# Kernel optimization log

Hardware: AMD Instinct MI355X
Metric: run time of the kernel (lower is better)

## Reference

```python
import jax, jax.numpy as jnp
import numpy as np

EPS = 0.5
MIN_SAMPLES = 5


def setup_inputs() -> dict:
    key = jax.random.key(0)
    X = jax.random.uniform(key, (12288, 8), dtype=jnp.float32)
    return {"X": X}


def reference(X):
    """DBSCAN: eps-range queries + cluster expansion, expressed as
    eps-graph connected components over core points (same clustering
    as the serial BFS in the original module; cluster ids are assigned
    in order of each cluster's minimum core index, matching the
    ascending-scan discovery order of the original)."""
    N = X.shape[0]
    SENTINEL = jnp.int32(N)

    # pairwise squared Euclidean distances [N, N] (KDTree range query equivalent)
    sq = jnp.sum(X * X, axis=1)
    d2 = sq[:, None] + sq[None, :] - 2.0 * (X @ X.T)
    adj = d2 <= (EPS * EPS)                      # eps-neighborhood (includes self)

    density = jnp.sum(adj, axis=1)               # |query_ball_point(x_i, eps)|
    core = density >= MIN_SAMPLES                # core-point mask

    # core-core edges: BFS expansion only propagates through cores
    core_adj = adj & core[None, :] & core[:, None]

    idx = jnp.arange(N, dtype=jnp.int32)
    init = jnp.where(core, idx, SENTINEL)        # each core starts as its own root

    def prop(lbl):
        # min label over core neighbors (min-plus propagation = connected components)
        nb_min = jnp.min(jnp.where(core_adj, lbl[None, :], SENTINEL), axis=1)
        return jnp.minimum(lbl, nb_min)

    def cond(state):
        cur, prev = state
        return jnp.any(cur != prev)

    def body(state):
        cur, _ = state
        return prop(cur), cur

    lbl, _ = jax.lax.while_loop(cond, body, (prop(init), init))

    # border points: non-core points within eps of a core join that core's cluster
    core_nb = jnp.min(jnp.where(adj & core[None, :], lbl[None, :], SENTINEL), axis=1)
    root = jnp.where(core, lbl, core_nb)         # SENTINEL -> noise

    # compact cluster ids: rank of each cluster root (min core index) ascending,
    # matching the original's sequential discovery order k = 0, 1, ...
    is_root = core & (lbl == idx)
    rank = jnp.cumsum(is_root.astype(jnp.int32)) - 1   # rank[i] valid where is_root[i]
    labels = jnp.where(root < SENTINEL,
                       rank[jnp.clip(root, 0, N - 1)],
                       jnp.int32(-1))
    return labels
```

## Files before the change

### kernel.cpp

```cpp
#include <hip/hip_runtime.h>

#define NPTS 12288
#define DIMS 8
#define EPS2 0.25f
#define MINS 5
#define NIB1 (NPTS / 256)
#define NW   (NPTS / 32)
#define SENT NPTS
#define RMAX 512
#define W    (RMAX / 32)
#define BIGL 0x3fffffff
#define FT   128
#define FB   256
#define FBGRID 256

#define ATHR 256
#define AROWS 2
#define ATI  (ATHR * AROWS)
#define AJC  128
#define AWCH (AJC / 32)
#define NJC  (NPTS / AJC)
#define NBLK 1200

typedef float v2f __attribute__((ext_vector_type(2)));

__device__ __forceinline__ float dot8(const v2f* xi, const float4& a, const float4& b) {
  v2f y0 = {a.x, a.y}, y1 = {a.z, a.w}, y2 = {b.x, b.y}, y3 = {b.z, b.w};
  v2f d = xi[0] * y0;
  d = __builtin_elementwise_fma(xi[1], y1, d);
  d = __builtin_elementwise_fma(xi[2], y2, d);
  d = __builtin_elementwise_fma(xi[3], y3, d);
  return d.x + d.y;
}

__device__ __forceinline__ unsigned int tr32(unsigned int x, int lane31) {
  const unsigned int M[5] = {0x0000FFFFu, 0x00FF00FFu, 0x0F0F0F0Fu,
                             0x33333333u, 0x55555555u};
  const int S[5] = {16, 8, 4, 2, 1};
#pragma unroll
  for (int k = 0; k < 5; ++k) {
    int s = S[k];
    unsigned int m = M[k];
    unsigned int p = __shfl_xor(x, s, 32);
    x = (lane31 & s) ? ((x & ~m) | ((p >> s) & m))
                     : ((x & m) | ((p & m) << s));
  }
  return x;
}


__global__ __launch_bounds__(ATHR) void k_adj(const float* __restrict__ X,
                                              unsigned int* __restrict__ adj,
                                              int* __restrict__ density) {
  __shared__ float4 xs[AJC][2];
  __shared__ float sqs[AJC];
  __shared__ unsigned int mir[AJC * 17];
  int t = threadIdx.x;

  int B = blockIdx.x;
  int bx = 0;
  while (2 * (bx + 1) * (48 - bx) <= B) bx++;
  int by = 4 * bx + (B - 2 * bx * (49 - bx));
  bool full = (by >= 4 * bx + 4);

  if (t < AJC) {
    int j = by * AJC + t;
    float4 a = ((const float4*)X)[j * 2];
    float4 b = ((const float4*)X)[j * 2 + 1];
    xs[t][0] = a; xs[t][1] = b;
    float sv = 0.f;
    sv = fmaf(a.x, a.x, sv); sv = fmaf(a.y, a.y, sv); sv = fmaf(a.z, a.z, sv); sv = fmaf(a.w, a.w, sv);
    sv = fmaf(b.x, b.x, sv); sv = fmaf(b.y, b.y, sv); sv = fmaf(b.z, b.z, sv); sv = fmaf(b.w, b.w, sv);
    sqs[t] = sv;
  }
  int i0 = bx * ATI + t, i1 = i0 + ATHR;
  v2f xi0[4], xi1[4];
  {
    float4 a0 = ((const float4*)X)[i0 * 2], b0v = ((const float4*)X)[i0 * 2 + 1];
    float4 a1 = ((const float4*)X)[i1 * 2], b1v = ((const float4*)X)[i1 * 2 + 1];
    xi0[0] = (v2f){a0.x, a0.y}; xi0[1] = (v2f){a0.z, a0.w};
    xi0[2] = (v2f){b0v.x, b0v.y}; xi0[3] = (v2f){b0v.z, b0v.w};
    xi1[0] = (v2f){a1.x, a1.y}; xi1[1] = (v2f){a1.z, a1.w};
    xi1[2] = (v2f){b1v.x, b1v.y}; xi1[3] = (v2f){b1v.z, b1v.w};
  }
  float sq0 = 0.f, sq1 = 0.f;
#pragma unroll
  for (int q = 0; q < 4; q++) {
    v2f p0 = xi0[q] * xi0[q], p1 = xi1[q] * xi1[q];
    sq0 += p0.x + p0.y; sq1 += p1.x + p1.y;
  }
  __syncthreads();
  unsigned int acc0[AWCH], acc1[AWCH];
#pragma unroll
  for (int w = 0; w < AWCH; w++) {
    unsigned int b0 = 0u, b1 = 0u;
#pragma unroll 4
    for (int bit = 0; bit < 32; bit++) {
      int jj = (w << 5) + bit;
      float4 xa = xs[jj][0], xb = xs[jj][1];
      float sj = sqs[jj];
      unsigned int m = 1u << bit;
      float d20 = (sq0 + sj) - 2.0f * dot8(xi0, xa, xb);
      float d21 = (sq1 + sj) - 2.0f * dot8(xi1, xa, xb);
      if (d20 <= EPS2) b0 |= m;
      if (d21 <= EPS2) b1 |= m;
    }
    acc0[w] = b0; acc1[w] = b1;
  }

  if (full) {
    *(uint4*)(adj + (size_t)i0 * NW + by * AWCH) = make_uint4(acc0[0], acc0[1], acc0[2], acc0[3]);
    *(uint4*)(adj + (size_t)i1 * NW + by * AWCH) = make_uint4(acc1[0], acc1[1], acc1[2], acc1[3]);
    int pc0 = 0, pc1 = 0;
#pragma unroll
    for (int w = 0; w < AWCH; w++) { pc0 += __popc(acc0[w]); pc1 += __popc(acc1[w]); }
    atomicAdd(&density[i0], pc0);
    atomicAdd(&density[i1], pc1);
  } else {
    int lw0 = min(max((i0 >> 5) - 4 * by, 0), 4);
    int lw1 = min(max((i1 >> 5) - 4 * by, 0), 4);
    unsigned int* dst0 = adj + (size_t)i0 * NW + by * AWCH;
    unsigned int* dst1 = adj + (size_t)i1 * NW + by * AWCH;
    int pc0 = 0, pc1 = 0;
    for (int wl = lw0; wl < AWCH; wl++) { dst0[wl] = acc0[wl]; pc0 += __popc(acc0[wl]); }
    for (int wl = lw1; wl < AWCH; wl++) { dst1[wl] = acc1[wl]; pc1 += __popc(acc1[wl]); }
    if (lw0 < AWCH) atomicAdd(&density[i0], pc0);
    if (lw1 < AWCH) atomicAdd(&density[i1], pc1);
  }

  const int lane31 = t & 31;
  const int g = t >> 5;
#pragma unroll
  for (int wl = 0; wl < AWCH; ++wl) {
    unsigned int x0 = tr32(acc0[wl], lane31);
    unsigned int x1 = tr32(acc1[wl], lane31);
    int rr = (wl << 5) + lane31;
    mir[rr * 17 + g] = x0;
    mir[rr * 17 + 8 + g] = x1;
  }
  __syncthreads();
  {
    int r = t >> 1, half = t & 1;
    int rglob = by * AJC + r;
    const unsigned int* mrow = &mir[r * 17 + half * 8];
    unsigned int* dstm = adj + (size_t)rglob * NW + bx * 16 + half * 8;
    if (full) {
      ((uint4*)dstm)[0] = make_uint4(mrow[0], mrow[1], mrow[2], mrow[3]);
      ((uint4*)dstm)[1] = make_uint4(mrow[4], mrow[5], mrow[6], mrow[7]);
      int pc = 0;
#pragma unroll
      for (int q = 0; q < 8; q++) pc += __popc(mrow[q]);
      atomicAdd(&density[rglob], pc);
    } else {
      int nv = min(max((rglob >> 5) - 16 * bx, 0), 16);
      int pc = 0, st = 0;
      for (int q = 0; q < 8; q++) {
        int qg = half * 8 + q;
        if (qg < nv) { dstm[q] = mrow[q]; pc += __popc(mrow[q]); st = 1; }
      }
      if (st) atomicAdd(&density[rglob], pc);
    }
  }
}

__global__ __launch_bounds__(256) void k_core(const int* __restrict__ density,
                                              unsigned long long* __restrict__ corebm,
                                              unsigned int* __restrict__ bm) {
  int t = threadIdx.x;
  if (blockIdx.x == 0) {
#pragma unroll
    for (int q = 0; q < RMAX * W / 256; q++) bm[t + q * 256] = 0u;
  }
  int i = blockIdx.x * 256 + t;
  unsigned long long m = __ballot(density[i] >= MINS);
  if ((t & 63) == 0) corebm[i >> 6] = m;
}

__global__ __launch_bounds__(64) void k_hookbm(const unsigned int* __restrict__ adj,
                                               const unsigned int* __restrict__ cb32,
                                               int* __restrict__ hook) {
  __shared__ unsigned int cb[NW];
  int t = threadIdx.x;
  for (int w = t; w < NW; w += 64) cb[w] = cb32[w];
  __syncthreads();
  int i = blockIdx.x * 64 + t;
  const unsigned int* row = adj + (size_t)i * NW;
  int wi = i >> 5;
  int m = i;
  for (int w = 0; w <= wi; w++) {
    unsigned int x = row[w] & cb[w];
    if (w == wi) x &= (1u << (i & 31)) - 1;
    if (x) { m = (w << 5) + __ffs(x) - 1; break; }
  }
  hook[i] = m;
}

__global__ __launch_bounds__(1024) void k_rid(const int* __restrict__ density,
                                              const int* __restrict__ hook,
                                              int* __restrict__ Rptr,
                                              int* __restrict__ labL,
                                              int* __restrict__ bcount) {
  __shared__ unsigned short ridS[NPTS];
  __shared__ int wsum[16];
  int t = threadIdx.x;
  int lane = t & 63, wid = t >> 6;
  const int SEG = NPTS / 1024;
  int base = t * SEG;
  int flags = 0;
  int s = 0;
#pragma unroll
  for (int k = 0; k < SEG; k++) {
    int i = base + k;
    int f = (density[i] >= MINS && hook[i] == i) ? 1 : 0;
    flags |= f << k;
    s += f;
  }
  int segsum = s;
#pragma unroll
  for (int off = 1; off < 64; off <<= 1) {
    int n = __shfl_up(s, off, 64);
    if (lane >= off) s += n;
  }
  if (lane == 63) wsum[wid] = s;
  __syncthreads();
  int woff = 0;
  for (int w = 0; w < wid; w++) woff += wsum[w];
  int run = woff + s - segsum;
#pragma unroll
  for (int k = 0; k < SEG; k++) {
    ridS[base + k] = (unsigned short)run;
    run += (flags >> k) & 1;
  }
  if (t == 1023) *Rptr = run;
  if (t == 0) *bcount = 0;
  __syncthreads();
  for (int k = 0; k < SEG; k++) {
    int i = base + k;
    int lab = -1;
    if (density[i] >= MINS) {
      int v = i, h = hook[v];
      while (h != v) { v = h; h = hook[v]; }
      lab = min((int)ridS[v], RMAX - 1);
    }
    labL[i] = lab;
  }
}

__global__ __launch_bounds__(FB) void k_fillbm(const unsigned int* __restrict__ adj,
                                               const unsigned int* __restrict__ cb32,
                                               const int* __restrict__ labL,
                                               unsigned int* __restrict__ bm) {
  __shared__ unsigned int bmL[RMAX * W];
  __shared__ unsigned short labS[NPTS];
  __shared__ unsigned int cb[NW];
  int t = threadIdx.x;
  for (int q = t; q < RMAX * W; q += FB) bmL[q] = 0u;
  for (int q = t; q < NPTS; q += FB) labS[q] = (unsigned short)(labL[q] + 1);
  for (int w = t; w < NW; w += FB) cb[w] = cb32[w];
  __syncthreads();
  int lane = t & 63, wv = t >> 6;
  int gw = blockIdx.x * 4 + wv;
  for (int i = gw; i < NPTS; i += 4 * FBGRID) {
    int a0 = (int)labS[i] - 1;
    if (a0 < 0) continue;
    const unsigned int* row = adj + (size_t)i * NW;
    int wi = i >> 5;
    for (int w = wi + lane; w < NW; w += 64) {
      unsigned int x = row[w] & cb[w];
      if (w == wi) x &= (0xFFFFFFFEu << (i & 31));
      while (x) {
        int b = __ffs(x) - 1; x &= x - 1;
        int lj = (int)labS[(w << 5) + b] - 1;
        if (lj != a0) {
          atomicOr(&bmL[a0 * W + (lj >> 5)], 1u << (lj & 31));
          atomicOr(&bmL[lj * W + (a0 >> 5)], 1u << (a0 & 31));
        }
      }
    }
  }
  __syncthreads();
  for (int q = t; q < RMAX * W; q += FB) {
    unsigned int v = bmL[q];
    if (v) atomicOr(&bm[q], v);
  }
}

__global__ __launch_bounds__(RMAX) void k_cc(const unsigned int* __restrict__ bm,
                                             const int* __restrict__ Rptr,
                                             int* __restrict__ clab) {
  __shared__ int lbl[RMAX];
  __shared__ int mn[RMAX];
  __shared__ int chg, cmp;
  int a = threadIdx.x;
  int R = *Rptr; if (R > RMAX) R = RMAX;
  lbl[a] = a;
  __syncthreads();
  while (true) {
    int m = lbl[a];
    if (a < R) {
      const unsigned int* row = bm + a * W;
#pragma unroll
      for (int w = 0; w < W; w++) {
        unsigned int bits = row[w];
        while (bits) {
          int b = __ffs(bits) - 1;
          bits &= bits - 1;
          m = min(m, lbl[(w << 5) + b]);
        }
      }
    }
    mn[a] = m;
    if (a == 0) chg = 0;
    __syncthreads();
    int l = lbl[a];
    if (m < l) { atomicMin(&lbl[l], m); atomicMin(&lbl[a], m); chg = 1; }
    __syncthreads();
    while (true) {
      if (a == 0) cmp = 0;
      __syncthreads();
      int nl = lbl[lbl[a]];
      __syncthreads();
      if (nl < lbl[a]) { lbl[a] = nl; cmp = 1; }
      __syncthreads();
      if (!cmp) break;
    }
    if (!chg) break;
    __syncthreads();
  }
  int flag = (a < R && lbl[a] == a) ? 1 : 0;
  mn[a] = flag;
  __syncthreads();
  for (int off = 1; off < RMAX; off <<= 1) {
    int v = mn[a];
    int add = (a >= off) ? mn[a - off] : 0;
    __syncthreads();
    mn[a] = v + add;
    __syncthreads();
  }
  clab[a] = mn[lbl[a]] - 1;
}

__global__ __launch_bounds__(256) void k_labels(const int* __restrict__ labL,
                                                const int* __restrict__ clab,
                                                int* __restrict__ labArr,
                                                int* __restrict__ blist,
                                                int* __restrict__ bcount,
                                                float* __restrict__ out) {
  int i = blockIdx.x * blockDim.x + threadIdx.x;
  if (i >= NPTS) return;
  int a = labL[i];
  if (a >= 0) {
    int lab = clab[a];
    labArr[i] = lab;
    out[i] = (float)lab;
  } else {
    labArr[i] = BIGL;
    out[i] = -1.0f;
    int pos = atomicAdd(bcount, 1);
    blist[pos] = i;
  }
}

__global__ __launch_bounds__(FT) void k_border(const unsigned int* __restrict__ adj,
                                               const unsigned int* __restrict__ cb32,
                                               const int* __restrict__ labArr,
                                               const int* __restrict__ blist,
                                               const int* __restrict__ bcount,
                                               float* __restrict__ out) {
  __shared__ unsigned int cb[NW];
  __shared__ int wm[FT / 64];
  int t = threadIdx.x;
  for (int w = t; w < NW; w += FT) cb[w] = cb32[w];
  __syncthreads();
  int count = *bcount;
  for (int k = blockIdx.x; k < count; k += gridDim.x) {
    int p = blist[k];
    const unsigned int* row = adj + (size_t)p * NW;
    int m = BIGL;
    for (int w = t; w < NW; w += FT) {
      unsigned int x = row[w] & cb[w];
      while (x) {
        int b = __ffs(x) - 1; x &= x - 1;
        m = min(m, labArr[(w << 5) + b]);
      }
    }
#pragma unroll
    for (int off = 32; off >= 1; off >>= 1) m = min(m, __shfl_xor(m, off, 64));
    if ((t & 63) == 0) wm[t >> 6] = m;
    __syncthreads();
    if (t == 0) {
      int mm = min(wm[0], wm[1]);
      out[p] = (mm < BIGL) ? (float)mm : -1.0f;
    }
    __syncthreads();
  }
}


extern "C" void kernel_launch(void* const* d_in, const int* in_sizes, int n_in,
                              void* d_out, int out_size, void* d_ws, size_t ws_size,
                              hipStream_t stream) {
  const float* X = (const float*)d_in[0];
  float* out = (float*)d_out;

  char* ws = (char*)d_ws;
  unsigned int* adj = (unsigned int*)ws;
  size_t off = (size_t)NPTS * NW * 4;
  int* density = (int*)(ws + off);           off += 4 * NPTS;
  int* hook    = (int*)(ws + off);           off += 4 * NPTS;
  int* labL    = (int*)(ws + off);           off += 4 * NPTS;
  int* labArr  = (int*)(ws + off);           off += 4 * NPTS;
  int* blist   = (int*)(ws + off);           off += 4 * NPTS;
  unsigned long long* corebm = (unsigned long long*)(ws + off); off += 2048;
  unsigned int* bm  = (unsigned int*)(ws + off); off += 4 * RMAX * W;
  int* clab    = (int*)(ws + off);           off += 4 * RMAX;
  int* Rptr    = (int*)(ws + off);
  int* bcount  = Rptr + 1;

  hipMemsetAsync(density, 0, 4 * NPTS, stream);

  k_adj<<<NBLK, ATHR, 0, stream>>>(X, adj, density);
  k_core<<<NIB1, 256, 0, stream>>>(density, corebm, bm);
  k_hookbm<<<NPTS / 64, 64, 0, stream>>>(adj, (const unsigned int*)corebm, hook);
  k_rid<<<1, 1024, 0, stream>>>(density, hook, Rptr, labL, bcount);
  k_fillbm<<<FBGRID, FB, 0, stream>>>(adj, (const unsigned int*)corebm, labL, bm);
  k_cc<<<1, RMAX, 0, stream>>>(bm, Rptr, clab);
  k_labels<<<NIB1, 256, 0, stream>>>(labL, clab, labArr, blist, bcount, out);
  k_border<<<256, FT, 0, stream>>>(adj, (const unsigned int*)corebm, labArr, blist, bcount, out);
}
```

Baseline: 207.3 us.

## Fuse core-mask into hook kernel and merge labels with border assignment

Removes k_core by having every hook block recompute the core bitmask from density into shared memory via ballots, with block 0 persisting it. The bm zeroing moves into the existing memset by placing bm contiguous with density. k_labels and k_border merge into one kernel that builds a per-block border list in shared memory and resolves border labels through clab[labL[...]] directly, dropping the labArr/blist/bcount global buffers. Two kernel launches go away, at the cost of redundant density reads in every hook block, one 256-thread block serially handling all of its own border points, and the fillbm grid being halved.

Measured after the change: 268.7 us. +29.6%, slower.

```diff
diff --git a/kernel.cpp b/kernel.cpp
--- a/kernel.cpp
+++ b/kernel.cpp
@@ -10,9 +10,8 @@
 #define RMAX 512
 #define W    (RMAX / 32)
 #define BIGL 0x3fffffff
-#define FT   128
 #define FB   256
-#define FBGRID 256
+#define FBGRID 128
 
 #define ATHR 256
 #define AROWS 2
@@ -163,25 +162,21 @@
   }
 }
 
-__global__ __launch_bounds__(256) void k_core(const int* __restrict__ density,
-                                              unsigned long long* __restrict__ corebm,
-                                              unsigned int* __restrict__ bm) {
-  int t = threadIdx.x;
-  if (blockIdx.x == 0) {
-#pragma unroll
-    for (int q = 0; q < RMAX * W / 256; q++) bm[t + q * 256] = 0u;
-  }
-  int i = blockIdx.x * 256 + t;
-  unsigned long long m = __ballot(density[i] >= MINS);
-  if ((t & 63) == 0) corebm[i >> 6] = m;
-}
-
-__global__ __launch_bounds__(64) void k_hookbm(const unsigned int* __restrict__ adj,
-                                               const unsigned int* __restrict__ cb32,
-                                               int* __restrict__ hook) {
+__global__ __launch_bounds__(64) void k_hookcore(const unsigned int* __restrict__ adj,
+                                                 const int* __restrict__ density,
+                                                 unsigned long long* __restrict__ corebm,
+                                                 int* __restrict__ hook) {
   __shared__ unsigned int cb[NW];
   int t = threadIdx.x;
-  for (int w = t; w < NW; w += 64) cb[w] = cb32[w];
+  bool persist = (blockIdx.x == 0);
+#pragma unroll 4
+  for (int q = 0; q < NPTS / 64; q++) {
+    unsigned long long m = __ballot(density[q * 64 + t] >= MINS);
+    if (t == 0) {
+      ((unsigned long long*)cb)[q] = m;
+      if (persist) corebm[q] = m;
+    }
+  }
   __syncthreads();
   int i = blockIdx.x * 64 + t;
   const unsigned int* row = adj + (size_t)i * NW;
@@ -198,8 +193,7 @@
 __global__ __launch_bounds__(1024) void k_rid(const int* __restrict__ density,
                                               const int* __restrict__ hook,
                                               int* __restrict__ Rptr,
-                                              int* __restrict__ labL,
-                                              int* __restrict__ bcount) {
+                                              int* __restrict__ labL) {
   __shared__ unsigned short ridS[NPTS];
   __shared__ int wsum[16];
   int t = threadIdx.x;
@@ -232,7 +226,6 @@
     run += (flags >> k) & 1;
   }
   if (t == 1023) *Rptr = run;
-  if (t == 0) *bcount = 0;
   __syncthreads();
   for (int k = 0; k < SEG; k++) {
     int i = base + k;
@@ -340,56 +333,46 @@
   clab[a] = mn[lbl[a]] - 1;
 }
 
-__global__ __launch_bounds__(256) void k_labels(const int* __restrict__ labL,
+__global__ __launch_bounds__(256) void k_labout(const unsigned int* __restrict__ adj,
+                                                const unsigned int* __restrict__ cb32,
+                                                const int* __restrict__ labL,
                                                 const int* __restrict__ clab,
-                                                int* __restrict__ labArr,
-                                                int* __restrict__ blist,
-                                                int* __restrict__ bcount,
                                                 float* __restrict__ out) {
-  int i = blockIdx.x * blockDim.x + threadIdx.x;
-  if (i >= NPTS) return;
+  __shared__ unsigned int cb[NW];
+  __shared__ int blistS[256];
+  __shared__ int bcnt;
+  __shared__ int wmn[4];
+  int t = threadIdx.x;
+  if (t == 0) bcnt = 0;
+  for (int w = t; w < NW; w += 256) cb[w] = cb32[w];
+  __syncthreads();
+  int i = blockIdx.x * 256 + t;
   int a = labL[i];
   if (a >= 0) {
-    int lab = clab[a];
-    labArr[i] = lab;
-    out[i] = (float)lab;
+    out[i] = (float)clab[a];
   } else {
-    labArr[i] = BIGL;
-    out[i] = -1.0f;
-    int pos = atomicAdd(bcount, 1);
-    blist[pos] = i;
-  }
-}
-
-__global__ __launch_bounds__(FT) void k_border(const unsigned int* __restrict__ adj,
-                                               const unsigned int* __restrict__ cb32,
-                                               const int* __restrict__ labArr,
-                                               const int* __restrict__ blist,
-                                               const int* __restrict__ bcount,
-                                               float* __restrict__ out) {
-  __shared__ unsigned int cb[NW];
-  __shared__ int wm[FT / 64];
-  int t = threadIdx.x;
-  for (int w = t; w < NW; w += FT) cb[w] = cb32[w];
-  __syncthreads();
-  int count = *bcount;
-  for (int k = blockIdx.x; k < count; k += gridDim.x) {
-    int p = blist[k];
+    int pos = atomicAdd(&bcnt, 1);
+    blistS[pos] = i;
+  }
+  __syncthreads();
+  int nb = bcnt;
+  for (int k = 0; k < nb; k++) {
+    int p = blistS[k];
     const unsigned int* row = adj + (size_t)p * NW;
     int m = BIGL;
-    for (int w = t; w < NW; w += FT) {
+    for (int w = t; w < NW; w += 256) {
       unsigned int x = row[w] & cb[w];
       while (x) {
         int b = __ffs(x) - 1; x &= x - 1;
-        m = min(m, labArr[(w << 5) + b]);
+        m = min(m, clab[labL[(w << 5) + b]]);
       }
     }
 #pragma unroll
     for (int off = 32; off >= 1; off >>= 1) m = min(m, __shfl_xor(m, off, 64));
-    if ((t & 63) == 0) wm[t >> 6] = m;
+    if ((t & 63) == 0) wmn[t >> 6] = m;
     __syncthreads();
     if (t == 0) {
-      int mm = min(wm[0], wm[1]);
+      int mm = min(min(wmn[0], wmn[1]), min(wmn[2], wmn[3]));
       out[p] = (mm < BIGL) ? (float)mm : -1.0f;
     }
     __syncthreads();
@@ -407,24 +390,19 @@
   unsigned int* adj = (unsigned int*)ws;
   size_t off = (size_t)NPTS * NW * 4;
   int* density = (int*)(ws + off);           off += 4 * NPTS;
+  unsigned int* bm  = (unsigned int*)(ws + off); off += 4 * RMAX * W;
   int* hook    = (int*)(ws + off);           off += 4 * NPTS;
   int* labL    = (int*)(ws + off);           off += 4 * NPTS;
-  int* labArr  = (int*)(ws + off);           off += 4 * NPTS;
-  int* blist   = (int*)(ws + off);           off += 4 * NPTS;
   unsigned long long* corebm = (unsigned long long*)(ws + off); off += 2048;
-  unsigned int* bm  = (unsigned int*)(ws + off); off += 4 * RMAX * W;
   int* clab    = (int*)(ws + off);           off += 4 * RMAX;
   int* Rptr    = (int*)(ws + off);
-  int* bcount  = Rptr + 1;
-
-  hipMemsetAsync(density, 0, 4 * NPTS, stream);
+
+  hipMemsetAsync(density, 0, 4 * NPTS + 4 * RMAX * W, stream);
 
   k_adj<<<NBLK, ATHR, 0, stream>>>(X, adj, density);
-  k_core<<<NIB1, 256, 0, stream>>>(density, corebm, bm);
-  k_hookbm<<<NPTS / 64, 64, 0, stream>>>(adj, (const unsigned int*)corebm, hook);
-  k_rid<<<1, 1024, 0, stream>>>(density, hook, Rptr, labL, bcount);
+  k_hookcore<<<NPTS / 64, 64, 0, stream>>>(adj, density, corebm, hook);
+  k_rid<<<1, 1024, 0, stream>>>(density, hook, Rptr, labL);
   k_fillbm<<<FBGRID, FB, 0, stream>>>(adj, (const unsigned int*)corebm, labL, bm);
   k_cc<<<1, RMAX, 0, stream>>>(bm, Rptr, clab);
-  k_labels<<<NIB1, 256, 0, stream>>>(labL, clab, labArr, blist, bcount, out);
-  k_border<<<256, FT, 0, stream>>>(adj, (const unsigned int*)corebm, labArr, blist, bcount, out);
-}
+  k_labout<<<NIB1, 256, 0, stream>>>(adj, (const unsigned int*)corebm, labL, clab, out);
+}
```
